# Performance work log

Hardware: AMD Instinct MI355X
Metric: run time of the kernel (lower is better)

## Reference

```python
import jax, jax.numpy as jnp
import numpy as np

N = 50000   # nodes
E = 800000  # edges (avg degree 16)
IN = 64     # in_dim
DS = 32     # in_dim // 2
HOUT = 64


def setup_inputs() -> dict:
    key = jax.random.key(0)
    ks = jax.random.split(key, 16)
    std = 0.1

    def w(k, shape):
        return std * jax.random.normal(k, shape, dtype=jnp.float32)

    z = lambda d: jnp.zeros((d,), dtype=jnp.float32)
    return {
        "x": jax.random.normal(ks[0], (N, IN), dtype=jnp.float32),
        "src": jax.random.randint(ks[1], (E,), 0, N),
        "dst": jax.random.randint(ks[2], (E,), 0, N),
        # encoders (enc_dim == in_dim branch: dim_split -> dim_split)
        "WencK": w(ks[3], (DS, DS)), "bencK": z(DS),
        "WencP1": w(ks[4], (DS, DS)), "bencP1": z(DS),
        "WencP2": w(ks[5], (DS, DS)), "bencP2": z(DS),
        # Kfun MLP: Linear(DS,HOUT) Tanh Linear(HOUT,HOUT) ReLU Linear(HOUT,HOUT)
        "WK1": w(ks[6], (DS, HOUT)), "bK1": z(HOUT),
        "WK2": w(ks[7], (HOUT, HOUT)), "bK2": z(HOUT),
        "WK3": w(ks[8], (HOUT, HOUT)), "bK3": z(HOUT),
        # Ufun MLP (same structure)
        "WU1": w(ks[9], (DS, HOUT)), "bU1": z(HOUT),
        "WU2": w(ks[10], (HOUT, HOUT)), "bU2": z(HOUT),
        "WU3": w(ks[11], (HOUT, HOUT)), "bU3": z(HOUT),
        # output heads
        "WH": w(ks[12], (HOUT, IN)), "bH": z(IN),
        "WD": w(ks[13], (IN, IN)), "bD": z(IN),
    }


def _mlp3(h, W1, b1, W2, b2, W3, b3):
    h = jnp.tanh(h @ W1 + b1)
    h = jax.nn.relu(h @ W2 + b2)
    return h @ W3 + b3


def reference(x, src, dst,
              WencK, bencK, WencP1, bencP1, WencP2, bencP2,
              WK1, bK1, WK2, bK2, WK3, bK3,
              WU1, bU1, WU2, bU2, WU3, bU3,
              WH, bH, WD, bD):
    ds = DS
    q, p = x[:, :ds], x[:, ds:]

    # getK: encode p, scatter-sum over incoming edges, node MLP
    hK = p @ WencK + bencK                              # [N, DS]
    hK_agg = jax.ops.segment_sum(hK[src], dst, num_segments=N)
    E_node = _mlp3(hK_agg, WK1, bK1, WK2, bK2, WK3, bK3)  # [N, HOUT]

    # getU: u_add_v on encoded q, edge MLP
    h1 = q @ WencP1 + bencP1
    h2 = q @ WencP2 + bencP2
    e_out = h1[src] + h2[dst]                           # [E, DS]
    E_edge = _mlp3(e_out, WU1, bU1, WU2, bU2, WU3, bU3)  # [E, HOUT]

    # getH: u_mul_e then sum into destination nodes
    E_new = jax.ops.segment_sum(E_node[src] * E_edge, dst, num_segments=N)

    # dHdx
    dH = E_new @ WH + bH                                # [N, IN]

    # get_D: dissipation term on second half of D(x), scattered over graph
    Dx = x @ WD + bD
    d_agg = jax.ops.segment_sum(Dx[:, ds:][src], dst, num_segments=N)
    d = jnp.concatenate([jnp.zeros_like(d_agg), d_agg], axis=-1)

    # dH @ J^T with J = [[0, I], [-I, 0]]  ->  [dH_p, -dH_q]
    out = jnp.concatenate([dH[:, ds:], -dH[:, :ds]], axis=-1) - d
    return out
```

## Files before the change

### kernel.cpp

```cpp
#include <hip/hip_runtime.h>
#include <hip/hip_bf16.h>

#define NN 50000
#define EE 800000
#define IN_DIM 64
#define DS_DIM 32
#define HOUT_DIM 64

#define K4_WAVES 10000
#define K4_EPW   80
#define K4_C     5
#define K4_NWG   (K4_WAVES / 4)

#define XA_EPW 64
#define XA_NWG 3125

#define HIST_BLOCKS 3125
#define ENC_BLOCKS  6250

#define SCAN_NB 196

#define XPS 72

typedef __attribute__((ext_vector_type(8))) short bf16x8;
typedef __attribute__((ext_vector_type(4))) float f32x4;

__device__ __forceinline__ float fast_tanh(float x) {
    float e = __builtin_amdgcn_exp2f(x * 2.885390082f);
    return 1.f - 2.f * __builtin_amdgcn_rcpf(e + 1.f);
}

__device__ __forceinline__ void atomAddF(float* p, float v) {
#if defined(__AMDGCN__)
    unsafeAtomicAdd(p, v);
#else
    atomicAdd(p, v);
#endif
}

__device__ __forceinline__ short f2b(float f) {
    union { __hip_bfloat16 h; short s; } u;
    u.h = __float2bfloat16(f);
    return u.s;
}
__device__ __forceinline__ float b2f(unsigned short u) {
    return __uint_as_float(((unsigned int)u) << 16);
}

__device__ __forceinline__ int xcd_swz(int bid, int nwg) {
    int xcd = bid & 7, idx = bid >> 3;
    int q = nwg >> 3, r = nwg & 7;
    return (xcd < r ? xcd * (q + 1) : r * (q + 1) + (xcd - r) * q) + idx;
}

__global__ void kmega0(const int* __restrict__ dst, int* __restrict__ cnt,
                       const float* __restrict__ x,
                       const float* __restrict__ WencP1, const float* __restrict__ bencP1,
                       const float* __restrict__ WencP2, const float* __restrict__ bencP2,
                       __hip_bfloat16* __restrict__ h1b, __hip_bfloat16* __restrict__ h2b,
                       __hip_bfloat16* __restrict__ xb) {
    if (blockIdx.x < HIST_BLOCKS) {
        int e = blockIdx.x * 256 + threadIdx.x;
        atomicAdd(&cnt[dst[e]], 1);
    } else {
        int tid = (blockIdx.x - HIST_BLOCKS) * 256 + threadIdx.x;
        int n = tid >> 5;
        int j = tid & 31;
        if (n >= NN) return;
        const float* xr = x + (size_t)n * IN_DIM;
        float a1 = bencP1[j], a2 = bencP2[j];
        #pragma unroll
        for (int k = 0; k < 32; k++) {
            float q = xr[k];
            a1 = fmaf(q, WencP1[k * 32 + j], a1);
            a2 = fmaf(q, WencP2[k * 32 + j], a2);
        }
        union { __hip_bfloat16 h; short s; } u1, u2, u3, u4;
        u1.s = f2b(a1); u2.s = f2b(a2);
        h1b[(size_t)n * 32 + j] = u1.h;
        h2b[(size_t)n * 32 + j] = u2.h;
        u3.s = f2b(xr[j]); u4.s = f2b(xr[32 + j]);
        xb[(size_t)n * 64 + j] = u3.h;
        xb[(size_t)n * 64 + 32 + j] = u4.h;
    }
}

__global__ void kscanA(const int* __restrict__ cnt, int* __restrict__ blocksum) {
    __shared__ int s[256];
    int t = threadIdx.x;
    int i = blockIdx.x * 256 + t;
    s[t] = (i < NN) ? cnt[i] : 0;
    __syncthreads();
    #pragma unroll
    for (int off = 128; off > 0; off >>= 1) {
        if (t < off) s[t] += s[t + off];
        __syncthreads();
    }
    if (t == 0) blocksum[blockIdx.x] = s[0];
}

__global__ void kscanB(const int* __restrict__ blocksum, int* __restrict__ blockoff) {
    __shared__ int part[256];
    int t = threadIdx.x;
    int v = (t < SCAN_NB) ? blocksum[t] : 0;
    part[t] = v;
    __syncthreads();
    for (int off = 1; off < 256; off <<= 1) {
        int u = (t >= off) ? part[t - off] : 0;
        __syncthreads();
        part[t] += u;
        __syncthreads();
    }
    if (t < SCAN_NB) blockoff[t] = part[t] - v;
}

__global__ void kscanC(const int* __restrict__ cnt, const int* __restrict__ blockoff,
                       int* __restrict__ rowptr) {
    __shared__ int part[256];
    int t = threadIdx.x;
    int i = blockIdx.x * 256 + t;
    int v = (i < NN) ? cnt[i] : 0;
    part[t] = v;
    __syncthreads();
    for (int off = 1; off < 256; off <<= 1) {
        int u = (t >= off) ? part[t - off] : 0;
        __syncthreads();
        part[t] += u;
        __syncthreads();
    }
    if (i < NN) {
        int incl = blockoff[blockIdx.x] + part[t];
        rowptr[i] = incl - v;
        if (i == NN - 1) rowptr[NN] = incl;
    }
}

__global__ void __launch_bounds__(256) kdfill(const int* __restrict__ rowptr,
                                              int* __restrict__ dstp) {
    int w = (blockIdx.x * blockDim.x + threadIdx.x) >> 6;
    int lane = threadIdx.x & 63;
    if (w >= NN) return;
    int lo = rowptr[w], hi = rowptr[w + 1];
    for (int p = lo + lane; p < hi; p += 64) dstp[p] = w;
}

__global__ void kscatter(const int* __restrict__ src, const int* __restrict__ dst,
                         const int* __restrict__ rowptr, int* __restrict__ fill,
                         int* __restrict__ srcp) {
    int e = blockIdx.x * 256 + threadIdx.x;
    if (e >= EE) return;
    int d = dst[e];
    int pos = rowptr[d] + atomicAdd(&fill[d], 1);
    srcp[pos] = src[e];
}

__global__ void __launch_bounds__(256) kxagg3(const int* __restrict__ srcp,
                                              const int* __restrict__ dstp,
                                              const __hip_bfloat16* __restrict__ xb,
                                              float* __restrict__ xagg) {
    int sbid = xcd_swz(blockIdx.x, XA_NWG);
    int w = sbid * 4 + (threadIdx.x >> 6);
    int lane = threadIdx.x & 63;
    int base = w * XA_EPW;
    const unsigned short* xu = reinterpret_cast<const unsigned short*>(xb);

    int sarr = srcp[base + lane];
    int darr = dstp[base + lane];

    float v0 = b2f(xu[(size_t)__shfl(sarr, 0) * 64 + lane]);
    float v1 = b2f(xu[(size_t)__shfl(sarr, 1) * 64 + lane]);
    float v2 = b2f(xu[(size_t)__shfl(sarr, 2) * 64 + lane]);
    float v3 = b2f(xu[(size_t)__shfl(sarr, 3) * 64 + lane]);
    int cd = __shfl(darr, 0);
    float carry = 0.f;

#define XA_STEP(vv, T)                                                        \
    {                                                                         \
        float cur = vv;                                                       \
        if ((T) + 4 < XA_EPW)                                                 \
            vv = b2f(xu[(size_t)__shfl(sarr, (T) + 4) * 64 + lane]);          \
        int d = __shfl(darr, (T));                                            \
        if (d != cd) {                                                        \
            atomAddF(&xagg[(size_t)cd * 64 + lane], carry);                   \
            cd = d; carry = 0.f;                                              \
        }                                                                     \
        carry += cur;                                                         \
    }

    for (int tb = 0; tb < XA_EPW; tb += 4) {
        XA_STEP(v0, tb);
        XA_STEP(v1, tb + 1);
        XA_STEP(v2, tb + 2);
        XA_STEP(v3, tb + 3);
    }
#undef XA_STEP
    atomAddF(&xagg[(size_t)cd * 64 + lane], carry);
}

__global__ void __launch_bounds__(256) k3ab(
    const float* __restrict__ xagg, const int* __restrict__ cnt,
    const float* __restrict__ WencK, const float* __restrict__ bencK,
    const float* __restrict__ WD, const float* __restrict__ bD,
    const float* __restrict__ WK1, const float* __restrict__ bK1,
    const float* __restrict__ WK2, const float* __restrict__ bK2,
    const float* __restrict__ WK3, const float* __restrict__ bK3,
    float* __restrict__ dagg, __hip_bfloat16* __restrict__ EnodeB)
{
    __shared__ unsigned short xpose[4][16 * XPS];
    const int wid  = threadIdx.x >> 6;
    const int lane = threadIdx.x & 63;
    const int g = lane >> 4;
    const int r = lane & 15;
    unsigned short* xp = xpose[wid];

    bf16x8 bwd[2][2];
    #pragma unroll
    for (int c = 0; c < 2; c++)
        #pragma unroll
        for (int nd = 0; nd < 2; nd++)
            #pragma unroll
            for (int i = 0; i < 8; i++)
                bwd[c][nd][i] = f2b(WD[(c * 32 + g * 8 + i) * 64 + 32 + nd * 16 + r]);
    bf16x8 bwk[2];
    #pragma unroll
    for (int nd = 0; nd < 2; nd++)
        #pragma unroll
        for (int i = 0; i < 8; i++)
            bwk[nd][i] = f2b(WencK[(g * 8 + i) * 32 + nd * 16 + r]);
    bf16x8 b1[4];
    #pragma unroll
    for (int nt = 0; nt < 4; nt++)
        #pragma unroll
        for (int i = 0; i < 8; i++)
            b1[nt][i] = f2b(WK1[(g * 8 + i) * 64 + nt * 16 + r]);
    bf16x8 b2[2][4], b3[2][4];
    #pragma unroll
    for (int c = 0; c < 2; c++)
        #pragma unroll
        for (int nt = 0; nt < 4; nt++)
            #pragma unroll
            for (int i = 0; i < 8; i++) {
                b2[c][nt][i] = f2b(WK2[(c * 32 + g * 8 + i) * 64 + nt * 16 + r]);
                b3[c][nt][i] = f2b(WK3[(c * 32 + g * 8 + i) * 64 + nt * 16 + r]);
            }
    float bdv[2], bkv[2];
    #pragma unroll
    for (int nd = 0; nd < 2; nd++) {
        bdv[nd] = bD[32 + nd * 16 + r];
        bkv[nd] = bencK[nd * 16 + r];
    }
    float bias1[4], bias2[4], bias3[4];
    #pragma unroll
    for (int nt = 0; nt < 4; nt++) {
        bias1[nt] = bK1[nt * 16 + r];
        bias2[nt] = bK2[nt * 16 + r];
        bias3[nt] = bK3[nt * 16 + r];
    }

    const int ntiles = NN / 16;
    const int wave = blockIdx.x * 4 + wid;
    const int nw = gridDim.x * 4;
    const f32x4 zero = {0.f, 0.f, 0.f, 0.f};

    for (int tile = wave; tile < ntiles; tile += nw) {
        bf16x8 ax0, ax1;
        {
            const float* xr = xagg + ((size_t)tile * 16 + r) * 64 + g * 8;
            float4 p0 = *reinterpret_cast<const float4*>(xr);
            float4 p1 = *reinterpret_cast<const float4*>(xr + 4);
            float4 p2 = *reinterpret_cast<const float4*>(xr + 32);
            float4 p3 = *reinterpret_cast<const float4*>(xr + 36);
            ax0[0] = f2b(p0.x); ax0[1] = f2b(p0.y); ax0[2] = f2b(p0.z); ax0[3] = f2b(p0.w);
            ax0[4] = f2b(p1.x); ax0[5] = f2b(p1.y); ax0[6] = f2b(p1.z); ax0[7] = f2b(p1.w);
            ax1[0] = f2b(p2.x); ax1[1] = f2b(p2.y); ax1[2] = f2b(p2.z); ax1[3] = f2b(p2.w);
            ax1[4] = f2b(p3.x); ax1[5] = f2b(p3.y); ax1[6] = f2b(p3.z); ax1[7] = f2b(p3.w);
        }
        float cq[4];
        #pragma unroll
        for (int q = 0; q < 4; q++) cq[q] = (float)cnt[tile * 16 + g * 4 + q];

        f32x4 accd[2];
        #pragma unroll
        for (int nd = 0; nd < 2; nd++) {
            accd[nd] = __builtin_amdgcn_mfma_f32_16x16x32_bf16(ax0, bwd[0][nd], zero, 0, 0, 0);
            accd[nd] = __builtin_amdgcn_mfma_f32_16x16x32_bf16(ax1, bwd[1][nd], accd[nd], 0, 0, 0);
        }
        #pragma unroll
        for (int nd = 0; nd < 2; nd++)
            #pragma unroll
            for (int q = 0; q < 4; q++)
                dagg[((size_t)tile * 16 + g * 4 + q) * 32 + nd * 16 + r] =
                    accd[nd][q] + cq[q] * bdv[nd];

        f32x4 acch[2];
        #pragma unroll
        for (int nd = 0; nd < 2; nd++)
            acch[nd] = __builtin_amdgcn_mfma_f32_16x16x32_bf16(ax1, bwk[nd], zero, 0, 0, 0);
        #pragma unroll
        for (int nd = 0; nd < 2; nd++)
            #pragma unroll
            for (int q = 0; q < 4; q++)
                xp[(g * 4 + q) * XPS + nd * 16 + r] = (unsigned short)f2b(acch[nd][q] + cq[q] * bkv[nd]);

        bf16x8 af = *reinterpret_cast<const bf16x8*>(xp + r * XPS + g * 8);
        f32x4 acc[4];
        #pragma unroll
        for (int nt = 0; nt < 4; nt++)
            acc[nt] = __builtin_amdgcn_mfma_f32_16x16x32_bf16(af, b1[nt], zero, 0, 0, 0);
        #pragma unroll
        for (int nt = 0; nt < 4; nt++)
            #pragma unroll
            for (int q = 0; q < 4; q++)
                xp[(g * 4 + q) * XPS + nt * 16 + r] = (unsigned short)f2b(fast_tanh(acc[nt][q] + bias1[nt]));

        f32x4 acc2[4] = {zero, zero, zero, zero};
        #pragma unroll
        for (int c = 0; c < 2; c++) {
            bf16x8 a2 = *reinterpret_cast<const bf16x8*>(xp + r * XPS + c * 32 + g * 8);
            #pragma unroll
            for (int nt = 0; nt < 4; nt++)
                acc2[nt] = __builtin_amdgcn_mfma_f32_16x16x32_bf16(a2, b2[c][nt], acc2[nt], 0, 0, 0);
        }
        #pragma unroll
        for (int nt = 0; nt < 4; nt++)
            #pragma unroll
            for (int q = 0; q < 4; q++)
                xp[(g * 4 + q) * XPS + nt * 16 + r] = (unsigned short)f2b(fmaxf(acc2[nt][q] + bias2[nt], 0.f));

        f32x4 acc3[4] = {zero, zero, zero, zero};
        #pragma unroll
        for (int c = 0; c < 2; c++) {
            bf16x8 a3 = *reinterpret_cast<const bf16x8*>(xp + r * XPS + c * 32 + g * 8);
            #pragma unroll
            for (int nt = 0; nt < 4; nt++)
                acc3[nt] = __builtin_amdgcn_mfma_f32_16x16x32_bf16(a3, b3[c][nt], acc3[nt], 0, 0, 0);
        }
        #pragma unroll
        for (int nt = 0; nt < 4; nt++)
            #pragma unroll
            for (int q = 0; q < 4; q++)
                xp[(g * 4 + q) * XPS + nt * 16 + r] = (unsigned short)f2b(acc3[nt][q] + bias3[nt]);
        {
            uint4 w0 = *reinterpret_cast<const uint4*>(xp + r * XPS + g * 16);
            uint4 w1 = *reinterpret_cast<const uint4*>(xp + r * XPS + g * 16 + 8);
            unsigned int* ob = reinterpret_cast<unsigned int*>(EnodeB + ((size_t)tile * 16 + r) * 64 + g * 16);
            *reinterpret_cast<uint4*>(ob) = w0;
            *reinterpret_cast<uint4*>(ob + 4) = w1;
        }
    }
}

__global__ void __launch_bounds__(256) k4_mfma(
    const int* __restrict__ srcp, const int* __restrict__ dstp,
    const __hip_bfloat16* __restrict__ h1b, const __hip_bfloat16* __restrict__ h2b,
    const __hip_bfloat16* __restrict__ EnodeB, float* __restrict__ Enew,
    const float* __restrict__ WU1, const float* __restrict__ bU1,
    const float* __restrict__ WU2, const float* __restrict__ bU2,
    const float* __restrict__ WU3, const float* __restrict__ bU3)
{
    __shared__ unsigned short xpose[4][16 * XPS];
    const int wid  = threadIdx.x >> 6;
    const int lane = threadIdx.x & 63;
    const int g = lane >> 4;
    const int r = lane & 15;
    unsigned short* xp = xpose[wid];

    bf16x8 b1[4];
    #pragma unroll
    for (int nt = 0; nt < 4; nt++) {
        #pragma unroll
        for (int i = 0; i < 8; i++)
            b1[nt][i] = f2b(WU1[(g * 8 + i) * 64 + nt * 16 + r]);
    }
    bf16x8 b2[2][4], b3[2][4];
    #pragma unroll
    for (int c = 0; c < 2; c++) {
        #pragma unroll
        for (int nt = 0; nt < 4; nt++) {
            #pragma unroll
            for (int i = 0; i < 8; i++) {
                b2[c][nt][i] = f2b(WU2[(c * 32 + g * 8 + i) * 64 + nt * 16 + r]);
                b3[c][nt][i] = f2b(WU3[(c * 32 + g * 8 + i) * 64 + nt * 16 + r]);
            }
        }
    }
    float bias1[4], bias2[4], bias3[4];
    #pragma unroll
    for (int nt = 0; nt < 4; nt++) {
        bias1[nt] = bU1[nt * 16 + r];
        bias2[nt] = bU2[nt * 16 + r];
        bias3[nt] = bU3[nt * 16 + r];
    }

    const int sbid = xcd_swz(blockIdx.x, K4_NWG);
    const int wave = sbid * 4 + wid;
    const int base = wave * K4_EPW;
    const f32x4 zero = {0.f, 0.f, 0.f, 0.f};
    const unsigned short* enB = reinterpret_cast<const unsigned short*>(EnodeB);

    int   cd[4] = {-1, -1, -1, -1};
    float cv0[4] = {0, 0, 0, 0}, cv1[4] = {0, 0, 0, 0},
          cv2[4] = {0, 0, 0, 0}, cv3[4] = {0, 0, 0, 0};

    int sp = srcp[base + r * K4_C];
    int dp = dstp[base + r * K4_C];
    uint4 v1 = *reinterpret_cast<const uint4*>(h1b + (size_t)sp * 32 + g * 8);
    uint4 v2 = *reinterpret_cast<const uint4*>(h2b + (size_t)dp * 32 + g * 8);

    for (int t = 0; t < K4_C; t++) {
        const int s_me = sp, d_me = dp;
        union { uint4 v; bf16x8 b; } ua1, ua2;
        ua1.v = v1; ua2.v = v2;
        if (t + 1 < K4_C) {
            sp = srcp[base + r * K4_C + t + 1];
            dp = dstp[base + r * K4_C + t + 1];
            v1 = *reinterpret_cast<const uint4*>(h1b + (size_t)sp * 32 + g * 8);
            v2 = *reinterpret_cast<const uint4*>(h2b + (size_t)dp * 32 + g * 8);
        }

        int dq[4];
        float en0[4], en1[4], en2[4], en3[4];
        #pragma unroll
        for (int q = 0; q < 4; q++) {
            const int er = g * 4 + q;
            const int ssv = __shfl(s_me, er);
            dq[q] = __shfl(d_me, er);
            const unsigned short* enp = enB + (size_t)ssv * 64 + r;
            en0[q] = b2f(enp[0]);
            en1[q] = b2f(enp[16]);
            en2[q] = b2f(enp[32]);
            en3[q] = b2f(enp[48]);
        }

        __builtin_amdgcn_s_setprio(1);
        f32x4 acc[4];
        #pragma unroll
        for (int nt = 0; nt < 4; nt++) {
            acc[nt] = __builtin_amdgcn_mfma_f32_16x16x32_bf16(ua2.b, b1[nt], zero, 0, 0, 0);
            acc[nt] = __builtin_amdgcn_mfma_f32_16x16x32_bf16(ua1.b, b1[nt], acc[nt], 0, 0, 0);
        }

        #pragma unroll
        for (int nt = 0; nt < 4; nt++) {
            #pragma unroll
            for (int q = 0; q < 4; q++)
                xp[(g * 4 + q) * XPS + nt * 16 + r] = (unsigned short)f2b(fast_tanh(acc[nt][q] + bias1[nt]));
        }

        f32x4 acc2[4] = {zero, zero, zero, zero};
        #pragma unroll
        for (int c = 0; c < 2; c++) {
            bf16x8 af = *reinterpret_cast<const bf16x8*>(xp + r * XPS + c * 32 + g * 8);
            #pragma unroll
            for (int nt = 0; nt < 4; nt++)
                acc2[nt] = __builtin_amdgcn_mfma_f32_16x16x32_bf16(af, b2[c][nt], acc2[nt], 0, 0, 0);
        }
        #pragma unroll
        for (int nt = 0; nt < 4; nt++) {
            #pragma unroll
            for (int q = 0; q < 4; q++)
                xp[(g * 4 + q) * XPS + nt * 16 + r] = (unsigned short)f2b(fmaxf(acc2[nt][q] + bias2[nt], 0.f));
        }

        f32x4 acc3[4] = {zero, zero, zero, zero};
        #pragma unroll
        for (int c = 0; c < 2; c++) {
            bf16x8 af = *reinterpret_cast<const bf16x8*>(xp + r * XPS + c * 32 + g * 8);
            #pragma unroll
            for (int nt = 0; nt < 4; nt++)
                acc3[nt] = __builtin_amdgcn_mfma_f32_16x16x32_bf16(af, b3[c][nt], acc3[nt], 0, 0, 0);
        }
        __builtin_amdgcn_s_setprio(0);

        #pragma unroll
        for (int q = 0; q < 4; q++) {
            float w0 = (acc3[0][q] + bias3[0]) * en0[q];
            float w1 = (acc3[1][q] + bias3[1]) * en1[q];
            float w2 = (acc3[2][q] + bias3[2]) * en2[q];
            float w3 = (acc3[3][q] + bias3[3]) * en3[q];
            if (dq[q] == cd[q]) {
                cv0[q] += w0; cv1[q] += w1; cv2[q] += w2; cv3[q] += w3;
            } else {
                if (cd[q] >= 0) {
                    float* ew = Enew + (size_t)cd[q] * 64 + r;
                    atomAddF(ew,      cv0[q]);
                    atomAddF(ew + 16, cv1[q]);
                    atomAddF(ew + 32, cv2[q]);
                    atomAddF(ew + 48, cv3[q]);
                }
                cd[q] = dq[q];
                cv0[q] = w0; cv1[q] = w1; cv2[q] = w2; cv3[q] = w3;
            }
        }
    }
    #pragma unroll
    for (int q = 0; q < 4; q++) {
        if (cd[q] >= 0) {
            float* ew = Enew + (size_t)cd[q] * 64 + r;
            atomAddF(ew,      cv0[q]);
            atomAddF(ew + 16, cv1[q]);
            atomAddF(ew + 32, cv2[q]);
            atomAddF(ew + 48, cv3[q]);
        }
    }
}

__global__ void k5_out(const float* __restrict__ Enew, const float* __restrict__ dagg,
                       const float* __restrict__ WH, const float* __restrict__ bH,
                       float* __restrict__ out) {
    int tid = blockIdx.x * blockDim.x + threadIdx.x;
    int n = tid >> 6;
    int j = tid & 63;
    if (n >= NN) return;
    const float* er = Enew + (size_t)n * 64;
    int jj = (j < 32) ? (j + 32) : (j - 32);
    float acc = bH[jj];
    #pragma unroll
    for (int k = 0; k < 64; k++) acc = fmaf(er[k], WH[k * 64 + jj], acc);
    float val;
    if (j < 32) val = acc;
    else        val = -acc - dagg[(size_t)n * 32 + (j - 32)];
    out[tid] = val;
}

extern "C" void kernel_launch(void* const* d_in, const int* in_sizes, int n_in,
                              void* d_out, int out_size, void* d_ws, size_t ws_size,
                              hipStream_t stream) {
    const float* x      = (const float*)d_in[0];
    const int*   src    = (const int*)d_in[1];
    const int*   dst    = (const int*)d_in[2];
    const float* WencK  = (const float*)d_in[3];
    const float* bencK  = (const float*)d_in[4];
    const float* WencP1 = (const float*)d_in[5];
    const float* bencP1 = (const float*)d_in[6];
    const float* WencP2 = (const float*)d_in[7];
    const float* bencP2 = (const float*)d_in[8];
    const float* WK1    = (const float*)d_in[9];
    const float* bK1    = (const float*)d_in[10];
    const float* WK2    = (const float*)d_in[11];
    const float* bK2    = (const float*)d_in[12];
    const float* WK3    = (const float*)d_in[13];
    const float* bK3    = (const float*)d_in[14];
    const float* WU1    = (const float*)d_in[15];
    const float* bU1    = (const float*)d_in[16];
    const float* WU2    = (const float*)d_in[17];
    const float* bU2    = (const float*)d_in[18];
    const float* WU3    = (const float*)d_in[19];
    const float* bU3    = (const float*)d_in[20];
    const float* WH     = (const float*)d_in[21];
    const float* bH     = (const float*)d_in[22];
    const float* WD     = (const float*)d_in[23];
    const float* bD     = (const float*)d_in[24];
    float* out = (float*)d_out;

    float* xagg = (float*)d_ws;
    float* Enew = xagg + (size_t)NN * 64;
    float* dagg = Enew + (size_t)NN * 64;
    __hip_bfloat16* h1b    = (__hip_bfloat16*)(dagg + (size_t)NN * 32);
    __hip_bfloat16* h2b    = h1b + (size_t)NN * 32;
    __hip_bfloat16* EnodeB = h2b + (size_t)NN * 32;
    __hip_bfloat16* xb     = EnodeB + (size_t)NN * 64;
    int*  cnt      = (int*)(xb + (size_t)NN * 64);
    int*  fill     = cnt + NN;
    int*  rowptr   = fill + NN;
    int*  blocksum = rowptr + NN + 2;
    int*  blockoff = blocksum + 256;
    int*  srcp     = blockoff + 256;
    int*  dstp     = srcp + EE;
    size_t need = (size_t)NN * 160 * 4 + (size_t)NN * 192 * 2
                + ((size_t)NN * 3 + 2 + 512) * 4 + (size_t)EE * 8;
    if (ws_size < need) return;

    hipMemsetAsync(cnt, 0, (size_t)2 * NN * sizeof(int), stream);
    hipMemsetAsync(xagg, 0, (size_t)NN * 128 * sizeof(float), stream);

    kmega0<<<HIST_BLOCKS + ENC_BLOCKS, 256, 0, stream>>>(
        dst, cnt, x, WencP1, bencP1, WencP2, bencP2, h1b, h2b, xb);
    kscanA<<<SCAN_NB, 256, 0, stream>>>(cnt, blocksum);
    kscanB<<<1, 256, 0, stream>>>(blocksum, blockoff);
    kscanC<<<SCAN_NB, 256, 0, stream>>>(cnt, blockoff, rowptr);
    kdfill<<<(NN * 64 + 255) / 256, 256, 0, stream>>>(rowptr, dstp);
    kscatter<<<HIST_BLOCKS, 256, 0, stream>>>(src, dst, rowptr, fill, srcp);
    kxagg3<<<XA_NWG, 256, 0, stream>>>(srcp, dstp, xb, xagg);
    k3ab<<<782, 256, 0, stream>>>(xagg, cnt, WencK, bencK, WD, bD,
                                  WK1, bK1, WK2, bK2, WK3, bK3, dagg, EnodeB);
    k4_mfma<<<K4_NWG, 256, 0, stream>>>(srcp, dstp, h1b, h2b, EnodeB, Enew,
                                        WU1, bU1, WU2, bU2, WU3, bU3);
    k5_out<<<(NN * 64 + 255) / 256, 256, 0, stream>>>(Enew, dagg, WH, bH, out);
}
```

Measured before the change: 294.9 us.

## Record atomic ranks in histogram, fold dst fill into scan, interleave Enode layout

The histogram pass now saves each edge's atomic rank, so the scatter no longer needs a second atomic counter and the fill array and its memset go away. The separate dst-fill kernel is merged into the scan kernel as a serial per-thread loop. Enode is stored in an interleaved column order so each lane in the edge kernel loads its four values with one 8-byte read, and Enew is permuted to match, with the output kernel undoing the permutation. This trades an extra E-sized rank array and a serial fill loop for fewer atomics, one fewer launch, and wider gathers.

Measured after the change: 369.0 us. 1.25x slower.

```diff
diff --git a/kernel.cpp b/kernel.cpp
--- a/kernel.cpp
+++ b/kernel.cpp
@@ -46,6 +46,9 @@
 __device__ __forceinline__ float b2f(unsigned short u) {
     return __uint_as_float(((unsigned int)u) << 16);
 }
+__device__ __forceinline__ unsigned int pack2(float lo, float hi) {
+    return (unsigned int)(unsigned short)f2b(lo) | (((unsigned int)(unsigned short)f2b(hi)) << 16);
+}
 
 __device__ __forceinline__ int xcd_swz(int bid, int nwg) {
     int xcd = bid & 7, idx = bid >> 3;
@@ -53,7 +56,7 @@
     return (xcd < r ? xcd * (q + 1) : r * (q + 1) + (xcd - r) * q) + idx;
 }
 
-__global__ void kmega0(const int* __restrict__ dst, int* __restrict__ cnt,
+__global__ void kmega0(const int* __restrict__ dst, int* __restrict__ cnt, int* __restrict__ rank,
                        const float* __restrict__ x,
                        const float* __restrict__ WencP1, const float* __restrict__ bencP1,
                        const float* __restrict__ WencP2, const float* __restrict__ bencP2,
@@ -61,7 +64,7 @@
                        __hip_bfloat16* __restrict__ xb) {
     if (blockIdx.x < HIST_BLOCKS) {
         int e = blockIdx.x * 256 + threadIdx.x;
-        atomicAdd(&cnt[dst[e]], 1);
+        rank[e] = atomicAdd(&cnt[dst[e]], 1);
     } else {
         int tid = (blockIdx.x - HIST_BLOCKS) * 256 + threadIdx.x;
         int n = tid >> 5;
@@ -115,7 +118,7 @@
 }
 
 __global__ void kscanC(const int* __restrict__ cnt, const int* __restrict__ blockoff,
-                       int* __restrict__ rowptr) {
+                       int* __restrict__ rowptr, int* __restrict__ dstp) {
     __shared__ int part[256];
     int t = threadIdx.x;
     int i = blockIdx.x * 256 + t;
@@ -130,28 +133,20 @@
     }
     if (i < NN) {
         int incl = blockoff[blockIdx.x] + part[t];
-        rowptr[i] = incl - v;
+        int lo = incl - v;
+        rowptr[i] = lo;
         if (i == NN - 1) rowptr[NN] = incl;
-    }
-}
-
-__global__ void __launch_bounds__(256) kdfill(const int* __restrict__ rowptr,
-                                              int* __restrict__ dstp) {
-    int w = (blockIdx.x * blockDim.x + threadIdx.x) >> 6;
-    int lane = threadIdx.x & 63;
-    if (w >= NN) return;
-    int lo = rowptr[w], hi = rowptr[w + 1];
-    for (int p = lo + lane; p < hi; p += 64) dstp[p] = w;
+        for (int p = lo; p < incl; p++) dstp[p] = i;
+    }
 }
 
 __global__ void kscatter(const int* __restrict__ src, const int* __restrict__ dst,
-                         const int* __restrict__ rowptr, int* __restrict__ fill,
+                         const int* __restrict__ rowptr, const int* __restrict__ rank,
                          int* __restrict__ srcp) {
     int e = blockIdx.x * 256 + threadIdx.x;
     if (e >= EE) return;
     int d = dst[e];
-    int pos = rowptr[d] + atomicAdd(&fill[d], 1);
-    srcp[pos] = src[e];
+    srcp[rowptr[d] + rank[e]] = src[e];
 }
 
 __global__ void __launch_bounds__(256) kxagg3(const int* __restrict__ srcp,
@@ -204,7 +199,7 @@
     const float* __restrict__ WK1, const float* __restrict__ bK1,
     const float* __restrict__ WK2, const float* __restrict__ bK2,
     const float* __restrict__ WK3, const float* __restrict__ bK3,
-    float* __restrict__ dagg, __hip_bfloat16* __restrict__ EnodeB)
+    float* __restrict__ dagg, __hip_bfloat16* __restrict__ EnodeT)
 {
     __shared__ unsigned short xpose[4][16 * XPS];
     const int wid  = threadIdx.x >> 6;
@@ -336,16 +331,12 @@
                 acc3[nt] = __builtin_amdgcn_mfma_f32_16x16x32_bf16(a3, b3[c][nt], acc3[nt], 0, 0, 0);
         }
         #pragma unroll
-        for (int nt = 0; nt < 4; nt++)
-            #pragma unroll
-            for (int q = 0; q < 4; q++)
-                xp[(g * 4 + q) * XPS + nt * 16 + r] = (unsigned short)f2b(acc3[nt][q] + bias3[nt]);
-        {
-            uint4 w0 = *reinterpret_cast<const uint4*>(xp + r * XPS + g * 16);
-            uint4 w1 = *reinterpret_cast<const uint4*>(xp + r * XPS + g * 16 + 8);
-            unsigned int* ob = reinterpret_cast<unsigned int*>(EnodeB + ((size_t)tile * 16 + r) * 64 + g * 16);
-            *reinterpret_cast<uint4*>(ob) = w0;
-            *reinterpret_cast<uint4*>(ob + 4) = w1;
+        for (int q = 0; q < 4; q++) {
+            uint2 v;
+            v.x = pack2(acc3[0][q] + bias3[0], acc3[1][q] + bias3[1]);
+            v.y = pack2(acc3[2][q] + bias3[2], acc3[3][q] + bias3[3]);
+            *reinterpret_cast<uint2*>(reinterpret_cast<unsigned short*>(EnodeT)
+                + ((size_t)tile * 16 + g * 4 + q) * 64 + r * 4) = v;
         }
     }
 }
@@ -353,7 +344,7 @@
 __global__ void __launch_bounds__(256) k4_mfma(
     const int* __restrict__ srcp, const int* __restrict__ dstp,
     const __hip_bfloat16* __restrict__ h1b, const __hip_bfloat16* __restrict__ h2b,
-    const __hip_bfloat16* __restrict__ EnodeB, float* __restrict__ Enew,
+    const __hip_bfloat16* __restrict__ EnodeT, float* __restrict__ Enew,
     const float* __restrict__ WU1, const float* __restrict__ bU1,
     const float* __restrict__ WU2, const float* __restrict__ bU2,
     const float* __restrict__ WU3, const float* __restrict__ bU3)
@@ -396,7 +387,7 @@
     const int wave = sbid * 4 + wid;
     const int base = wave * K4_EPW;
     const f32x4 zero = {0.f, 0.f, 0.f, 0.f};
-    const unsigned short* enB = reinterpret_cast<const unsigned short*>(EnodeB);
+    const unsigned short* enT = reinterpret_cast<const unsigned short*>(EnodeT);
 
     int   cd[4] = {-1, -1, -1, -1};
     float cv0[4] = {0, 0, 0, 0}, cv1[4] = {0, 0, 0, 0},
@@ -425,11 +416,11 @@
             const int er = g * 4 + q;
             const int ssv = __shfl(s_me, er);
             dq[q] = __shfl(d_me, er);
-            const unsigned short* enp = enB + (size_t)ssv * 64 + r;
-            en0[q] = b2f(enp[0]);
-            en1[q] = b2f(enp[16]);
-            en2[q] = b2f(enp[32]);
-            en3[q] = b2f(enp[48]);
+            uint2 ev = *reinterpret_cast<const uint2*>(enT + (size_t)ssv * 64 + r * 4);
+            en0[q] = b2f((unsigned short)(ev.x & 0xffff));
+            en1[q] = b2f((unsigned short)(ev.x >> 16));
+            en2[q] = b2f((unsigned short)(ev.y & 0xffff));
+            en3[q] = b2f((unsigned short)(ev.y >> 16));
         }
 
         __builtin_amdgcn_s_setprio(1);
@@ -482,11 +473,11 @@
                 cv0[q] += w0; cv1[q] += w1; cv2[q] += w2; cv3[q] += w3;
             } else {
                 if (cd[q] >= 0) {
-                    float* ew = Enew + (size_t)cd[q] * 64 + r;
-                    atomAddF(ew,      cv0[q]);
-                    atomAddF(ew + 16, cv1[q]);
-                    atomAddF(ew + 32, cv2[q]);
-                    atomAddF(ew + 48, cv3[q]);
+                    float* ew = Enew + (size_t)cd[q] * 64 + r * 4;
+                    atomAddF(ew,     cv0[q]);
+                    atomAddF(ew + 1, cv1[q]);
+                    atomAddF(ew + 2, cv2[q]);
+                    atomAddF(ew + 3, cv3[q]);
                 }
                 cd[q] = dq[q];
                 cv0[q] = w0; cv1[q] = w1; cv2[q] = w2; cv3[q] = w3;
@@ -496,11 +487,11 @@
     #pragma unroll
     for (int q = 0; q < 4; q++) {
         if (cd[q] >= 0) {
-            float* ew = Enew + (size_t)cd[q] * 64 + r;
-            atomAddF(ew,      cv0[q]);
-            atomAddF(ew + 16, cv1[q]);
-            atomAddF(ew + 32, cv2[q]);
-            atomAddF(ew + 48, cv3[q]);
+            float* ew = Enew + (size_t)cd[q] * 64 + r * 4;
+            atomAddF(ew,     cv0[q]);
+            atomAddF(ew + 1, cv1[q]);
+            atomAddF(ew + 2, cv2[q]);
+            atomAddF(ew + 3, cv3[q]);
         }
     }
 }
@@ -516,7 +507,10 @@
     int jj = (j < 32) ? (j + 32) : (j - 32);
     float acc = bH[jj];
     #pragma unroll
-    for (int k = 0; k < 64; k++) acc = fmaf(er[k], WH[k * 64 + jj], acc);
+    for (int k = 0; k < 64; k++) {
+        int p = (k & 15) * 4 + (k >> 4);
+        acc = fmaf(er[p], WH[k * 64 + jj], acc);
+    }
     float val;
     if (j < 32) val = acc;
     else        val = -acc - dagg[(size_t)n * 32 + (j - 32)];
@@ -558,33 +552,32 @@
     float* dagg = Enew + (size_t)NN * 64;
     __hip_bfloat16* h1b    = (__hip_bfloat16*)(dagg + (size_t)NN * 32);
     __hip_bfloat16* h2b    = h1b + (size_t)NN * 32;
-    __hip_bfloat16* EnodeB = h2b + (size_t)NN * 32;
-    __hip_bfloat16* xb     = EnodeB + (size_t)NN * 64;
+    __hip_bfloat16* EnodeT = h2b + (size_t)NN * 32;
+    __hip_bfloat16* xb     = EnodeT + (size_t)NN * 64;
     int*  cnt      = (int*)(xb + (size_t)NN * 64);
-    int*  fill     = cnt + NN;
-    int*  rowptr   = fill + NN;
+    int*  rowptr   = cnt + NN;
     int*  blocksum = rowptr + NN + 2;
     int*  blockoff = blocksum + 256;
-    int*  srcp     = blockoff + 256;
+    int*  rank     = blockoff + 256;
+    int*  srcp     = rank + EE;
     int*  dstp     = srcp + EE;
     size_t need = (size_t)NN * 160 * 4 + (size_t)NN * 192 * 2
-                + ((size_t)NN * 3 + 2 + 512) * 4 + (size_t)EE * 8;
+                + ((size_t)NN * 2 + 2 + 512) * 4 + (size_t)EE * 12;
     if (ws_size < need) return;
 
-    hipMemsetAsync(cnt, 0, (size_t)2 * NN * sizeof(int), stream);
+    hipMemsetAsync(cnt, 0, (size_t)NN * sizeof(int), stream);
     hipMemsetAsync(xagg, 0, (size_t)NN * 128 * sizeof(float), stream);
 
     kmega0<<<HIST_BLOCKS + ENC_BLOCKS, 256, 0, stream>>>(
-        dst, cnt, x, WencP1, bencP1, WencP2, bencP2, h1b, h2b, xb);
+        dst, cnt, rank, x, WencP1, bencP1, WencP2, bencP2, h1b, h2b, xb);
     kscanA<<<SCAN_NB, 256, 0, stream>>>(cnt, blocksum);
     kscanB<<<1, 256, 0, stream>>>(blocksum, blockoff);
-    kscanC<<<SCAN_NB, 256, 0, stream>>>(cnt, blockoff, rowptr);
-    kdfill<<<(NN * 64 + 255) / 256, 256, 0, stream>>>(rowptr, dstp);
-    kscatter<<<HIST_BLOCKS, 256, 0, stream>>>(src, dst, rowptr, fill, srcp);
+    kscanC<<<SCAN_NB, 256, 0, stream>>>(cnt, blockoff, rowptr, dstp);
+    kscatter<<<HIST_BLOCKS, 256, 0, stream>>>(src, dst, rowptr, rank, srcp);
     kxagg3<<<XA_NWG, 256, 0, stream>>>(srcp, dstp, xb, xagg);
     k3ab<<<782, 256, 0, stream>>>(xagg, cnt, WencK, bencK, WD, bD,
-                                  WK1, bK1, WK2, bK2, WK3, bK3, dagg, EnodeB);
-    k4_mfma<<<K4_NWG, 256, 0, stream>>>(srcp, dstp, h1b, h2b, EnodeB, Enew,
+                                  WK1, bK1, WK2, bK2, WK3, bK3, dagg, EnodeT);
+    k4_mfma<<<K4_NWG, 256, 0, stream>>>(srcp, dstp, h1b, h2b, EnodeT, Enew,
                                         WU1, bU1, WU2, bU2, WU3, bU3);
     k5_out<<<(NN * 64 + 255) / 256, 256, 0, stream>>>(Enew, dagg, WH, bH, out);
 }
```
